# Kernel optimization log

Measured on AMD Instinct MI355X. Metric: run time of the kernel, lower is better.

The kernel has to match this reference:

```python
import jax, jax.numpy as jnp
import numpy as np

N_EMBD = 1024
VOCAB = 64
B, T = 8, 4096


def setup_inputs() -> dict:
    key = jax.random.key(0)
    ks = jax.random.split(key, 6)
    x = jax.random.normal(ks[0], (B, T, N_EMBD), dtype=jnp.float32)
    idx = jax.random.randint(ks[1], (B, T), 0, VOCAB, dtype=jnp.int64)
    emb_weight = jax.random.normal(ks[2], (VOCAB, N_EMBD), dtype=jnp.float32)
    head_weight = jax.random.normal(ks[3], (VOCAB, N_EMBD), dtype=jnp.float32)
    gate = jax.random.normal(ks[4], (1, 1, N_EMBD), dtype=jnp.float32) * 0.01
    soft_gate = jax.random.normal(ks[5], (1, 1, N_EMBD), dtype=jnp.float32) * 0.01
    return {"x": x, "idx": idx, "emb_weight": emb_weight,
            "head_weight": head_weight, "gate": gate, "soft_gate": soft_gate}


def reference(x, idx, emb_weight, head_weight, gate, soft_gate):
    # --- idx-gated codebook blend (idx from previous step's argmax, clamped >= 0) ---
    idx_c = jnp.clip(idx, 0, None)
    emb = emb_weight[idx_c]                                  # [B,T,D]
    g = jax.nn.sigmoid(x * gate).mean(axis=-1, keepdims=True)  # [B,T,1]
    x = x * (1.0 - g) + emb * g
    # (tmix/cmix are external and treated as identity here)
    # --- small-vocab head + softmax-weighted codebook lookup ---
    logits = jnp.einsum('btd,vd->btv', x, head_weight)        # [B,T,64]
    soft_prob = jax.nn.softmax(logits, axis=-1)
    soft_emb = jnp.einsum('btv,vd->btd', soft_prob, emb_weight)
    sg = jax.nn.sigmoid(x * soft_gate).mean(axis=-1, keepdims=True)
    x = x * (1.0 - sg) + soft_emb * sg
    # --- argmax indexing for next step ---
    new_idx = jnp.argmax(logits, axis=-1)                     # [B,T]
    return x, new_idx
```

## Files before the change

### kernel.cpp

```cpp
#include <hip/hip_runtime.h>
#include <hip/hip_bf16.h>


#define DIMS 1024
#define VOCAB 64
#define NTOK 32768
#define TTILE 16
#define TPB 512
#define IDX_OFF (NTOK * DIMS)
#define CAND_DELTA 2.5f

typedef __attribute__((ext_vector_type(8))) short short8;
typedef __attribute__((ext_vector_type(4))) float f32x4;

__device__ __forceinline__ float sigm(float z) {
    return __builtin_amdgcn_rcpf(1.f + __expf(-z));
}
__device__ __forceinline__ unsigned short f2bf(float f) {
    __hip_bfloat16 h = __float2bfloat16(f);
    return *reinterpret_cast<unsigned short*>(&h);
}
__device__ __forceinline__ float bf2f(unsigned short u) {
    __hip_bfloat16 h = *reinterpret_cast<__hip_bfloat16*>(&u);
    return __bfloat162float(h);
}

__global__ void prep_weights(const float* __restrict__ head,
                             const float* __restrict__ emb,
                             __hip_bfloat16* __restrict__ headB,
                             __hip_bfloat16* __restrict__ embT) {
    int t = blockIdx.x * 256 + threadIdx.x;
    int v = t >> 10, d = t & 1023;
    headB[t] = __float2bfloat16(head[t]);
    embT[d * VOCAB + v] = __float2bfloat16(emb[v * DIMS + d]);
}

__global__ __launch_bounds__(TPB) void fused_block(
    const float* __restrict__ x,
    const int* __restrict__ idx,
    const float* __restrict__ emb,
    const float* __restrict__ gate,
    const float* __restrict__ sgate,
    const float* __restrict__ headF,
    const __hip_bfloat16* __restrict__ headB,
    const __hip_bfloat16* __restrict__ embT,
    float* __restrict__ out)
{
    __shared__ __align__(16) __hip_bfloat16 sX1b[TTILE][1032];
    __shared__ __align__(16) float          sLogP[TTILE][68];
    __shared__ __align__(16) __hip_bfloat16 sP[TTILE][72];
    __shared__ float sSg[TTILE];

    const int tid  = threadIdx.x;
    const int tk   = tid >> 5;
    const int l32  = tid & 31;
    const long t0  = (long)blockIdx.x * TTILE;
    const long tok = t0 + tk;

    float4 xv[8];
    float gsum = 0.f;
    int ic = idx[tok]; if (ic < 0) ic = 0;
    const float4* xrow = (const float4*)(x + tok * DIMS);
    const float4* grow = (const float4*)gate;
    #pragma unroll
    for (int c = 0; c < 8; c++) {
        int f = l32 + c * 32;
        float4 v = xrow[f];
        float4 gv = grow[f];
        xv[c] = v;
        gsum += sigm(v.x * gv.x) + sigm(v.y * gv.y)
              + sigm(v.z * gv.z) + sigm(v.w * gv.w);
    }
    gsum += __shfl_xor(gsum, 1); gsum += __shfl_xor(gsum, 2);
    gsum += __shfl_xor(gsum, 4); gsum += __shfl_xor(gsum, 8);
    gsum += __shfl_xor(gsum, 16);
    const float g = gsum * (1.f / 1024.f);

    const float4* erow = (const float4*)(emb + (long)ic * DIMS);
    const float4* srow = (const float4*)sgate;
    float ssum = 0.f;
    #pragma unroll
    for (int c = 0; c < 8; c++) {
        int f = l32 + c * 32;
        float4 ev = erow[f];
        float4 sv = srow[f];
        float4 a;
        a.x = xv[c].x * (1.f - g) + ev.x * g;
        a.y = xv[c].y * (1.f - g) + ev.y * g;
        a.z = xv[c].z * (1.f - g) + ev.z * g;
        a.w = xv[c].w * (1.f - g) + ev.w * g;
        xv[c] = a;
        ssum += sigm(a.x * sv.x) + sigm(a.y * sv.y)
              + sigm(a.z * sv.z) + sigm(a.w * sv.w);
        ushort4 pk;
        pk.x = f2bf(a.x); pk.y = f2bf(a.y); pk.z = f2bf(a.z); pk.w = f2bf(a.w);
        *(ushort4*)&sX1b[tk][f * 4] = pk;
    }
    ssum += __shfl_xor(ssum, 1); ssum += __shfl_xor(ssum, 2);
    ssum += __shfl_xor(ssum, 4); ssum += __shfl_xor(ssum, 8);
    ssum += __shfl_xor(ssum, 16);
    if (l32 == 0) sSg[tk] = ssum * (1.f / 1024.f);
    __syncthreads();

    const int w    = tid >> 6;
    const int lane = tid & 63;
    const int quad = lane >> 4, l16 = lane & 15;
    if (w < 4) {
        f32x4 acc0 = {0.f, 0.f, 0.f, 0.f};
        f32x4 acc1 = {0.f, 0.f, 0.f, 0.f};
        const __hip_bfloat16* hrow = headB + (long)(w * 16 + l16) * DIMS + quad * 8;
        #pragma unroll 2
        for (int k0 = 0; k0 < 1024; k0 += 64) {
            short8 a0 = *(const short8*)&sX1b[l16][k0 + quad * 8];
            short8 b0 = *(const short8*)(hrow + k0);
            acc0 = __builtin_amdgcn_mfma_f32_16x16x32_bf16(a0, b0, acc0, 0, 0, 0);
            short8 a1 = *(const short8*)&sX1b[l16][k0 + 32 + quad * 8];
            short8 b1 = *(const short8*)(hrow + k0 + 32);
            acc1 = __builtin_amdgcn_mfma_f32_16x16x32_bf16(a1, b1, acc1, 0, 0, 0);
        }
        #pragma unroll
        for (int i = 0; i < 4; i++)
            sLogP[quad * 4 + i][w * 16 + l16] = acc0[i] + acc1[i];
    }
    __syncthreads();

    unsigned long long candA, candB;
    {
        float lA = sLogP[2 * w][lane];
        float lB = sLogP[2 * w + 1][lane];
        float mA = lA, mB = lB;
        #pragma unroll
        for (int k = 1; k < 64; k <<= 1) {
            mA = fmaxf(mA, __shfl_xor(mA, k));
            mB = fmaxf(mB, __shfl_xor(mB, k));
        }
        float eA = __expf(lA - mA), eB = __expf(lB - mB);
        float sA = eA, sB = eB;
        #pragma unroll
        for (int k = 1; k < 64; k <<= 1) {
            sA += __shfl_xor(sA, k);
            sB += __shfl_xor(sB, k);
        }
        sP[2 * w][lane]     = __float2bfloat16(eA * __builtin_amdgcn_rcpf(sA));
        sP[2 * w + 1][lane] = __float2bfloat16(eB * __builtin_amdgcn_rcpf(sB));
        candA = __ballot(lA >= mA - CAND_DELTA);
        candB = __ballot(lB >= mB - CAND_DELTA);
    }

    {
        unsigned long long cm = ((lane >> 5) & 1) ? candB : candA;
        int bi;
        if (__popcll(cm) == 1) {
            bi = __ffsll(cm) - 1;
        } else {
            float bv = -3.4e38f; bi = 0;
            while (cm) {
                int v = __ffsll(cm) - 1;
                cm &= cm - 1;
                const float4* hr = (const float4*)(headF + (long)v * DIMS);
                float p = 0.f;
                #pragma unroll
                for (int c = 0; c < 8; c++) {
                    float4 hv = hr[l32 + c * 32];
                    p = fmaf(xv[c].x, hv.x, p); p = fmaf(xv[c].y, hv.y, p);
                    p = fmaf(xv[c].z, hv.z, p); p = fmaf(xv[c].w, hv.w, p);
                }
                p += __shfl_xor(p, 1); p += __shfl_xor(p, 2);
                p += __shfl_xor(p, 4); p += __shfl_xor(p, 8);
                p += __shfl_xor(p, 16);
                if (p > bv) { bv = p; bi = v; }
            }
        }
        if (l32 == 0) out[IDX_OFF + tok] = (float)bi;
    }
    __syncthreads();

    {
        const float sg = sSg[l16];
        short8 pb0 = *(const short8*)&sP[l16][quad * 8];
        short8 pb1 = *(const short8*)&sP[l16][32 + quad * 8];
        float* orow = out + (t0 + l16) * (long)DIMS + quad * 4;
        #pragma unroll 2
        for (int i = 0; i < 8; i++) {
            int n0 = (i * 8 + w) * 16;
            const __hip_bfloat16* er = embT + (long)(n0 + l16) * VOCAB + quad * 8;
            f32x4 acc = {0.f, 0.f, 0.f, 0.f};
            acc = __builtin_amdgcn_mfma_f32_16x16x32_bf16(*(const short8*)er, pb0, acc, 0, 0, 0);
            acc = __builtin_amdgcn_mfma_f32_16x16x32_bf16(*(const short8*)(er + 32), pb1, acc, 0, 0, 0);
            ushort4 xb = *(const ushort4*)&sX1b[l16][n0 + quad * 4];
            float4 o;
            o.x = bf2f(xb.x) * (1.f - sg) + acc[0] * sg;
            o.y = bf2f(xb.y) * (1.f - sg) + acc[1] * sg;
            o.z = bf2f(xb.z) * (1.f - sg) + acc[2] * sg;
            o.w = bf2f(xb.w) * (1.f - sg) + acc[3] * sg;
            *(float4*)(orow + n0) = o;
        }
    }
}

extern "C" void kernel_launch(void* const* d_in, const int* in_sizes, int n_in,
                              void* d_out, int out_size, void* d_ws, size_t ws_size,
                              hipStream_t stream) {
    const float* xp    = (const float*)d_in[0];
    const int*   idxp  = (const int*)d_in[1];
    const float* embp  = (const float*)d_in[2];
    const float* headp = (const float*)d_in[3];
    const float* gp    = (const float*)d_in[4];
    const float* sgp   = (const float*)d_in[5];
    float*       outp  = (float*)d_out;

    __hip_bfloat16* headB = (__hip_bfloat16*)d_ws;
    __hip_bfloat16* embT  = (__hip_bfloat16*)((char*)d_ws + 131072);

    prep_weights<<<dim3(256), dim3(256), 0, stream>>>(headp, embp, headB, embT);
    fused_block<<<dim3(NTOK / TTILE), dim3(TPB), 0, stream>>>(
        xp, idxp, embp, gp, sgp, headp, headB, embT, outp);
}
```

Before: 296.6 us.

## Restructure fused kernel to one wavefront per 16-token tile without LDS staging

Replaces the 512-thread block (16 tokens, LDS-staged bf16 activations, block-wide barriers) with a single 64-lane wavefront per 16 tokens. The wave computes the logits directly from register-built MFMA A-fragments, does softmax and argmax candidate selection in registers, and rereads x and emb from global memory in the output pass instead of keeping a bf16 copy. The aim is to remove block-level synchronization and most LDS traffic, and to raise occupancy. The cost is that x and emb rows are read three times from global memory and cache, and each wave runs a longer serial loop over the full hidden dimension.

```diff
diff --git a/kernel.cpp b/kernel.cpp
--- a/kernel.cpp
+++ b/kernel.cpp
@@ -5,8 +5,6 @@
 #define DIMS 1024
 #define VOCAB 64
 #define NTOK 32768
-#define TTILE 16
-#define TPB 512
 #define IDX_OFF (NTOK * DIMS)
 #define CAND_DELTA 2.5f
 
@@ -19,10 +17,6 @@
 __device__ __forceinline__ unsigned short f2bf(float f) {
     __hip_bfloat16 h = __float2bfloat16(f);
     return *reinterpret_cast<unsigned short*>(&h);
-}
-__device__ __forceinline__ float bf2f(unsigned short u) {
-    __hip_bfloat16 h = *reinterpret_cast<__hip_bfloat16*>(&u);
-    return __bfloat162float(h);
 }
 
 __global__ void prep_weights(const float* __restrict__ head,
@@ -35,7 +29,7 @@
     embT[d * VOCAB + v] = __float2bfloat16(emb[v * DIMS + d]);
 }
 
-__global__ __launch_bounds__(TPB) void fused_block(
+__global__ __launch_bounds__(64) void fused_wave(
     const float* __restrict__ x,
     const int* __restrict__ idx,
     const float* __restrict__ emb,
@@ -46,154 +40,159 @@
     const __hip_bfloat16* __restrict__ embT,
     float* __restrict__ out)
 {
-    __shared__ __align__(16) __hip_bfloat16 sX1b[TTILE][1032];
-    __shared__ __align__(16) float          sLogP[TTILE][68];
-    __shared__ __align__(16) __hip_bfloat16 sP[TTILE][72];
-    __shared__ float sSg[TTILE];
-
-    const int tid  = threadIdx.x;
-    const int tk   = tid >> 5;
-    const int l32  = tid & 31;
-    const long t0  = (long)blockIdx.x * TTILE;
-    const long tok = t0 + tk;
-
-    float4 xv[8];
+    __shared__ __align__(16) __hip_bfloat16 sP[16][72];
+
+    const int lane = threadIdx.x;
+    const int quad = lane >> 4, l16 = lane & 15;
+    const long t0w  = (long)blockIdx.x * 16;
+    const long tokL = t0w + l16;
+    const float* xrowL = x + tokL * DIMS;
+
     float gsum = 0.f;
-    int ic = idx[tok]; if (ic < 0) ic = 0;
-    const float4* xrow = (const float4*)(x + tok * DIMS);
-    const float4* grow = (const float4*)gate;
+    #pragma unroll 4
+    for (int c = 0; c < 32; c++) {
+        int off = c * 32 + quad * 8;
+        float4 v0 = *(const float4*)(xrowL + off);
+        float4 v1 = *(const float4*)(xrowL + off + 4);
+        float4 g0 = *(const float4*)(gate + off);
+        float4 g1 = *(const float4*)(gate + off + 4);
+        gsum += sigm(v0.x*g0.x) + sigm(v0.y*g0.y) + sigm(v0.z*g0.z) + sigm(v0.w*g0.w)
+              + sigm(v1.x*g1.x) + sigm(v1.y*g1.y) + sigm(v1.z*g1.z) + sigm(v1.w*g1.w);
+    }
+    gsum += __shfl_xor(gsum, 16);
+    gsum += __shfl_xor(gsum, 32);
+    const float g = gsum * (1.f / 1024.f);
+
+    int ic = idx[tokL]; if (ic < 0) ic = 0;
+    const float* erowL = emb + (long)ic * DIMS;
+
+    f32x4 acc0 = {0.f,0.f,0.f,0.f}, acc1 = {0.f,0.f,0.f,0.f};
+    f32x4 acc2 = {0.f,0.f,0.f,0.f}, acc3 = {0.f,0.f,0.f,0.f};
+    float ssum = 0.f;
+    const __hip_bfloat16* hb = headB + (long)l16 * DIMS;
+    #pragma unroll 2
+    for (int c = 0; c < 32; c++) {
+        int off = c * 32 + quad * 8;
+        float4 v0 = *(const float4*)(xrowL + off);
+        float4 v1 = *(const float4*)(xrowL + off + 4);
+        float4 e0 = *(const float4*)(erowL + off);
+        float4 e1 = *(const float4*)(erowL + off + 4);
+        float4 s0 = *(const float4*)(sgate + off);
+        float4 s1 = *(const float4*)(sgate + off + 4);
+        float a0 = v0.x*(1.f-g) + e0.x*g, a1 = v0.y*(1.f-g) + e0.y*g;
+        float a2 = v0.z*(1.f-g) + e0.z*g, a3 = v0.w*(1.f-g) + e0.w*g;
+        float a4 = v1.x*(1.f-g) + e1.x*g, a5 = v1.y*(1.f-g) + e1.y*g;
+        float a6 = v1.z*(1.f-g) + e1.z*g, a7 = v1.w*(1.f-g) + e1.w*g;
+        ssum += sigm(a0*s0.x) + sigm(a1*s0.y) + sigm(a2*s0.z) + sigm(a3*s0.w)
+              + sigm(a4*s1.x) + sigm(a5*s1.y) + sigm(a6*s1.z) + sigm(a7*s1.w);
+        short8 af;
+        af[0] = (short)f2bf(a0); af[1] = (short)f2bf(a1);
+        af[2] = (short)f2bf(a2); af[3] = (short)f2bf(a3);
+        af[4] = (short)f2bf(a4); af[5] = (short)f2bf(a5);
+        af[6] = (short)f2bf(a6); af[7] = (short)f2bf(a7);
+        short8 b0 = *(const short8*)(hb + off);
+        short8 b1 = *(const short8*)(hb + 16 * DIMS + off);
+        short8 b2 = *(const short8*)(hb + 32 * DIMS + off);
+        short8 b3 = *(const short8*)(hb + 48 * DIMS + off);
+        acc0 = __builtin_amdgcn_mfma_f32_16x16x32_bf16(af, b0, acc0, 0, 0, 0);
+        acc1 = __builtin_amdgcn_mfma_f32_16x16x32_bf16(af, b1, acc1, 0, 0, 0);
+        acc2 = __builtin_amdgcn_mfma_f32_16x16x32_bf16(af, b2, acc2, 0, 0, 0);
+        acc3 = __builtin_amdgcn_mfma_f32_16x16x32_bf16(af, b3, acc3, 0, 0, 0);
+    }
+    ssum += __shfl_xor(ssum, 16);
+    ssum += __shfl_xor(ssum, 32);
+    const float sg = ssum * (1.f / 1024.f);
+
+    unsigned long long cand[4];
     #pragma unroll
-    for (int c = 0; c < 8; c++) {
-        int f = l32 + c * 32;
-        float4 v = xrow[f];
-        float4 gv = grow[f];
-        xv[c] = v;
-        gsum += sigm(v.x * gv.x) + sigm(v.y * gv.y)
-              + sigm(v.z * gv.z) + sigm(v.w * gv.w);
-    }
-    gsum += __shfl_xor(gsum, 1); gsum += __shfl_xor(gsum, 2);
-    gsum += __shfl_xor(gsum, 4); gsum += __shfl_xor(gsum, 8);
-    gsum += __shfl_xor(gsum, 16);
-    const float g = gsum * (1.f / 1024.f);
-
-    const float4* erow = (const float4*)(emb + (long)ic * DIMS);
-    const float4* srow = (const float4*)sgate;
-    float ssum = 0.f;
-    #pragma unroll
-    for (int c = 0; c < 8; c++) {
-        int f = l32 + c * 32;
-        float4 ev = erow[f];
-        float4 sv = srow[f];
-        float4 a;
-        a.x = xv[c].x * (1.f - g) + ev.x * g;
-        a.y = xv[c].y * (1.f - g) + ev.y * g;
-        a.z = xv[c].z * (1.f - g) + ev.z * g;
-        a.w = xv[c].w * (1.f - g) + ev.w * g;
-        xv[c] = a;
-        ssum += sigm(a.x * sv.x) + sigm(a.y * sv.y)
-              + sigm(a.z * sv.z) + sigm(a.w * sv.w);
-        ushort4 pk;
-        pk.x = f2bf(a.x); pk.y = f2bf(a.y); pk.z = f2bf(a.z); pk.w = f2bf(a.w);
-        *(ushort4*)&sX1b[tk][f * 4] = pk;
-    }
-    ssum += __shfl_xor(ssum, 1); ssum += __shfl_xor(ssum, 2);
-    ssum += __shfl_xor(ssum, 4); ssum += __shfl_xor(ssum, 8);
-    ssum += __shfl_xor(ssum, 16);
-    if (l32 == 0) sSg[tk] = ssum * (1.f / 1024.f);
-    __syncthreads();
-
-    const int w    = tid >> 6;
-    const int lane = tid & 63;
-    const int quad = lane >> 4, l16 = lane & 15;
-    if (w < 4) {
-        f32x4 acc0 = {0.f, 0.f, 0.f, 0.f};
-        f32x4 acc1 = {0.f, 0.f, 0.f, 0.f};
-        const __hip_bfloat16* hrow = headB + (long)(w * 16 + l16) * DIMS + quad * 8;
-        #pragma unroll 2
-        for (int k0 = 0; k0 < 1024; k0 += 64) {
-            short8 a0 = *(const short8*)&sX1b[l16][k0 + quad * 8];
-            short8 b0 = *(const short8*)(hrow + k0);
-            acc0 = __builtin_amdgcn_mfma_f32_16x16x32_bf16(a0, b0, acc0, 0, 0, 0);
-            short8 a1 = *(const short8*)&sX1b[l16][k0 + 32 + quad * 8];
-            short8 b1 = *(const short8*)(hrow + k0 + 32);
-            acc1 = __builtin_amdgcn_mfma_f32_16x16x32_bf16(a1, b1, acc1, 0, 0, 0);
-        }
-        #pragma unroll
-        for (int i = 0; i < 4; i++)
-            sLogP[quad * 4 + i][w * 16 + l16] = acc0[i] + acc1[i];
-    }
-    __syncthreads();
-
-    unsigned long long candA, candB;
+    for (int i = 0; i < 4; i++) {
+        float m = fmaxf(fmaxf(acc0[i], acc1[i]), fmaxf(acc2[i], acc3[i]));
+        m = fmaxf(m, __shfl_xor(m, 1));
+        m = fmaxf(m, __shfl_xor(m, 2));
+        m = fmaxf(m, __shfl_xor(m, 4));
+        m = fmaxf(m, __shfl_xor(m, 8));
+        float e0 = __expf(acc0[i] - m), e1 = __expf(acc1[i] - m);
+        float e2 = __expf(acc2[i] - m), e3 = __expf(acc3[i] - m);
+        float s = e0 + e1 + e2 + e3;
+        s += __shfl_xor(s, 1); s += __shfl_xor(s, 2);
+        s += __shfl_xor(s, 4); s += __shfl_xor(s, 8);
+        float rs = __builtin_amdgcn_rcpf(s);
+        int mr = quad * 4 + i;
+        sP[mr][ 0 + l16] = __float2bfloat16(e0 * rs);
+        sP[mr][16 + l16] = __float2bfloat16(e1 * rs);
+        sP[mr][32 + l16] = __float2bfloat16(e2 * rs);
+        sP[mr][48 + l16] = __float2bfloat16(e3 * rs);
+        unsigned long long b0 = __ballot(acc0[i] >= m - CAND_DELTA);
+        unsigned long long b1 = __ballot(acc1[i] >= m - CAND_DELTA);
+        unsigned long long b2 = __ballot(acc2[i] >= m - CAND_DELTA);
+        unsigned long long b3 = __ballot(acc3[i] >= m - CAND_DELTA);
+        int sh = quad * 16;
+        cand[i] = ((b0 >> sh) & 0xFFFFull)
+                | (((b1 >> sh) & 0xFFFFull) << 16)
+                | (((b2 >> sh) & 0xFFFFull) << 32)
+                | (((b3 >> sh) & 0xFFFFull) << 48);
+    }
+
     {
-        float lA = sLogP[2 * w][lane];
-        float lB = sLogP[2 * w + 1][lane];
-        float mA = lA, mB = lB;
-        #pragma unroll
-        for (int k = 1; k < 64; k <<= 1) {
-            mA = fmaxf(mA, __shfl_xor(mA, k));
-            mB = fmaxf(mB, __shfl_xor(mB, k));
-        }
-        float eA = __expf(lA - mA), eB = __expf(lB - mB);
-        float sA = eA, sB = eB;
-        #pragma unroll
-        for (int k = 1; k < 64; k <<= 1) {
-            sA += __shfl_xor(sA, k);
-            sB += __shfl_xor(sB, k);
-        }
-        sP[2 * w][lane]     = __float2bfloat16(eA * __builtin_amdgcn_rcpf(sA));
-        sP[2 * w + 1][lane] = __float2bfloat16(eB * __builtin_amdgcn_rcpf(sB));
-        candA = __ballot(lA >= mA - CAND_DELTA);
-        candB = __ballot(lB >= mB - CAND_DELTA);
-    }
-
-    {
-        unsigned long long cm = ((lane >> 5) & 1) ? candB : candA;
+        int srcl = (l16 >> 2) * 16;
+        unsigned long long m0 = __shfl(cand[0], srcl);
+        unsigned long long m1 = __shfl(cand[1], srcl);
+        unsigned long long m2 = __shfl(cand[2], srcl);
+        unsigned long long m3 = __shfl(cand[3], srcl);
+        int s = l16 & 3;
+        unsigned long long cm = (s == 0) ? m0 : (s == 1) ? m1 : (s == 2) ? m2 : m3;
         int bi;
         if (__popcll(cm) == 1) {
             bi = __ffsll(cm) - 1;
         } else {
+            const float* xr  = xrowL + quad * 256;
+            const float* er2 = erowL + quad * 256;
             float bv = -3.4e38f; bi = 0;
             while (cm) {
                 int v = __ffsll(cm) - 1;
                 cm &= cm - 1;
-                const float4* hr = (const float4*)(headF + (long)v * DIMS);
+                const float* hr = headF + (long)v * DIMS + quad * 256;
                 float p = 0.f;
-                #pragma unroll
-                for (int c = 0; c < 8; c++) {
-                    float4 hv = hr[l32 + c * 32];
-                    p = fmaf(xv[c].x, hv.x, p); p = fmaf(xv[c].y, hv.y, p);
-                    p = fmaf(xv[c].z, hv.z, p); p = fmaf(xv[c].w, hv.w, p);
+                #pragma unroll 4
+                for (int c4 = 0; c4 < 64; c4++) {
+                    float4 xv4 = *(const float4*)(xr  + c4 * 4);
+                    float4 ev4 = *(const float4*)(er2 + c4 * 4);
+                    float4 hv4 = *(const float4*)(hr  + c4 * 4);
+                    p = fmaf(xv4.x*(1.f-g) + ev4.x*g, hv4.x, p);
+                    p = fmaf(xv4.y*(1.f-g) + ev4.y*g, hv4.y, p);
+                    p = fmaf(xv4.z*(1.f-g) + ev4.z*g, hv4.z, p);
+                    p = fmaf(xv4.w*(1.f-g) + ev4.w*g, hv4.w, p);
                 }
-                p += __shfl_xor(p, 1); p += __shfl_xor(p, 2);
-                p += __shfl_xor(p, 4); p += __shfl_xor(p, 8);
                 p += __shfl_xor(p, 16);
+                p += __shfl_xor(p, 32);
                 if (p > bv) { bv = p; bi = v; }
             }
         }
-        if (l32 == 0) out[IDX_OFF + tok] = (float)bi;
-    }
+        if (quad == 0) out[IDX_OFF + tokL] = (float)bi;
+    }
+
     __syncthreads();
 
     {
-        const float sg = sSg[l16];
         short8 pb0 = *(const short8*)&sP[l16][quad * 8];
         short8 pb1 = *(const short8*)&sP[l16][32 + quad * 8];
-        float* orow = out + (t0 + l16) * (long)DIMS + quad * 4;
+        float* orow = out + tokL * DIMS;
+        const __hip_bfloat16* ebase = embT + (long)l16 * VOCAB + quad * 8;
         #pragma unroll 2
-        for (int i = 0; i < 8; i++) {
-            int n0 = (i * 8 + w) * 16;
-            const __hip_bfloat16* er = embT + (long)(n0 + l16) * VOCAB + quad * 8;
-            f32x4 acc = {0.f, 0.f, 0.f, 0.f};
-            acc = __builtin_amdgcn_mfma_f32_16x16x32_bf16(*(const short8*)er, pb0, acc, 0, 0, 0);
-            acc = __builtin_amdgcn_mfma_f32_16x16x32_bf16(*(const short8*)(er + 32), pb1, acc, 0, 0, 0);
-            ushort4 xb = *(const ushort4*)&sX1b[l16][n0 + quad * 4];
+        for (int i = 0; i < 64; i++) {
+            int n0 = i * 16;
+            const __hip_bfloat16* er = ebase + (long)n0 * VOCAB;
+            f32x4 a2 = {0.f, 0.f, 0.f, 0.f};
+            a2 = __builtin_amdgcn_mfma_f32_16x16x32_bf16(*(const short8*)er,        pb0, a2, 0, 0, 0);
+            a2 = __builtin_amdgcn_mfma_f32_16x16x32_bf16(*(const short8*)(er + 32), pb1, a2, 0, 0, 0);
+            float4 xb = *(const float4*)(xrowL + n0 + quad * 4);
+            float4 eb = *(const float4*)(erowL + n0 + quad * 4);
             float4 o;
-            o.x = bf2f(xb.x) * (1.f - sg) + acc[0] * sg;
-            o.y = bf2f(xb.y) * (1.f - sg) + acc[1] * sg;
-            o.z = bf2f(xb.z) * (1.f - sg) + acc[2] * sg;
-            o.w = bf2f(xb.w) * (1.f - sg) + acc[3] * sg;
-            *(float4*)(orow + n0) = o;
+            float x1x = xb.x*(1.f-g) + eb.x*g;  o.x = x1x*(1.f-sg) + a2[0]*sg;
+            float x1y = xb.y*(1.f-g) + eb.y*g;  o.y = x1y*(1.f-sg) + a2[1]*sg;
+            float x1z = xb.z*(1.f-g) + eb.z*g;  o.z = x1z*(1.f-sg) + a2[2]*sg;
+            float x1w = xb.w*(1.f-g) + eb.w*g;  o.w = x1w*(1.f-sg) + a2[3]*sg;
+            *(float4*)(orow + n0 + quad * 4) = o;
         }
     }
 }
@@ -213,6 +212,6 @@
     __hip_bfloat16* embT  = (__hip_bfloat16*)((char*)d_ws + 131072);
 
     prep_weights<<<dim3(256), dim3(256), 0, stream>>>(headp, embp, headB, embT);
-    fused_block<<<dim3(NTOK / TTILE), dim3(TPB), 0, stream>>>(
+    fused_wave<<<dim3(NTOK / 16), dim3(64), 0, stream>>>(
         xp, idxp, embp, gp, sgp, headp, headB, embT, outp);
 }
```

Measured after the change: 403.2 us. 1.36x slower.
